# Kernel optimization log

Hardware: AMD Instinct MI355X
Metric: run time of the kernel (lower is better)

## Reference

```python
import jax, jax.numpy as jnp
import numpy as np

PATCH_NUMS = (1, 2, 4, 8, 16)
BETA = 0.25
A = -0.75  # torch bicubic coefficient


def _cubic(s):
    s = abs(s)
    if s <= 1.0:
        return ((A + 2.0) * s - (A + 3.0)) * s * s + 1.0
    if s < 2.0:
        return (((s - 5.0) * s + 8.0) * s - 4.0) * A
    return 0.0


def bicubic_matrix(n_in, n_out):
    # Row-stochastic 1D resampling matrix matching torch upsample_bicubic2d
    # (align_corners=False: half-pixel centers, border index clamping).
    scale = n_in / n_out
    W = np.zeros((n_out, n_in), dtype=np.float32)
    for i in range(n_out):
        x = (i + 0.5) * scale - 0.5
        x0 = int(np.floor(x))
        t = x - x0
        for off in (-1, 0, 1, 2):
            idx = min(max(x0 + off, 0), n_in - 1)
            W[i, idx] += _cubic(t - off)
    return jnp.asarray(W)


def area_down(x, pn):
    # exact average pooling (h, w divisible by pn)
    b, c, h, w = x.shape
    kh, kw = h // pn, w // pn
    return x.reshape(b, c, pn, kh, pn, kw).mean(axis=(3, 5))


def bicubic_up(x, h_out, w_out):
    b, c, h_in, w_in = x.shape
    Wh = bicubic_matrix(h_in, h_out)  # (h_out, h_in)
    Ww = bicubic_matrix(w_in, w_out)  # (w_out, w_in)
    x = jnp.einsum('Oh,bchw->bcOw', Wh, x)
    x = jnp.einsum('Pw,bchw->bchP', Ww, x)
    return x


def vector_quantize(z, embed, beta):
    # z: (b,c,h,w); embed: (V,c)
    b, c, h, w = z.shape
    zf = z.transpose(0, 2, 3, 1).reshape(-1, c)  # (N,c)
    # squared L2 distances to codebook, (N,V)
    d = (zf * zf).sum(-1, keepdims=True) - 2.0 * zf @ embed.T + (embed * embed).sum(-1)
    idx = jnp.argmin(d, axis=1)  # (N,)
    zq = embed[idx].reshape(b, h, w, c).transpose(0, 3, 1, 2)
    sg = jax.lax.stop_gradient
    loss = beta * jnp.mean((sg(zq) - z) ** 2) + jnp.mean((zq - sg(z)) ** 2)
    zq_st = z + sg(zq - z)  # straight-through estimator
    return zq_st, idx.reshape(b, h, w), loss


def setup_inputs() -> dict:
    key = jax.random.key(0)
    k1, k2 = jax.random.split(key)
    z = jax.random.normal(k1, (256, 32, 16, 16), dtype=jnp.float32)
    embed = jax.random.normal(k2, (4096, 32), dtype=jnp.float32)
    return {"z": z, "embed": embed}


def reference(z, embed):
    b, c, h, w = z.shape
    f_rest = z
    f_hat = jnp.zeros_like(z)
    ms_idx = []
    vq_loss = jnp.float32(0.0)
    n = len(PATCH_NUMS)
    for i, pn in enumerate(PATCH_NUMS):
        z_scale = area_down(f_rest, pn) if i < n - 1 else f_rest
        z_q_scale, idx, loss_i = vector_quantize(z_scale, embed, BETA)
        z_q = bicubic_up(z_q_scale, h, w) if i < n - 1 else z_q_scale
        f_hat = f_hat + z_q
        f_rest = f_rest - z_q
        ms_idx.append(idx)
        vq_loss = vq_loss + loss_i
    vq_loss = vq_loss / n
    return (f_hat, *ms_idx, vq_loss)
```

## Files before the change

kernel.cpp:

```cpp
#include <hip/hip_runtime.h>
#include <hip/hip_bf16.h>
#include <cstdint>
#include <cstddef>


#define B_   256
#define V_   4096
#define NTOT 2097152
#define WIN  128
#define CAP  512
#define ZS   65536

using bf16x8 = __attribute__((ext_vector_type(8))) short;
using f32x4  = __attribute__((ext_vector_type(4))) float;

__device__ inline short f2bf(float f) {
  __hip_bfloat16 h = __float2bfloat16(f);
  return *reinterpret_cast<short*>(&h);
}
__device__ inline unsigned encf(float f) {
  unsigned u = __float_as_uint(f);
  return (u & 0x80000000u) ? ~u : (u | 0x80000000u);
}
__device__ inline float decf(unsigned u) {
  unsigned b = (u & 0x80000000u) ? (u ^ 0x80000000u) : ~u;
  return __uint_as_float(b);
}
__device__ inline int keyidx(unsigned long long k) {
  int i = (int)(unsigned)(k & 0xffffffffull);
  return min(max(i, 0), V_ - 1);
}

__global__ __launch_bounds__(256) void setup_kernel(
    const float* __restrict__ z, const float* __restrict__ embed,
    float* __restrict__ f_rest, float* __restrict__ zpack,
    short* __restrict__ ebf, float* __restrict__ se,
    float* __restrict__ tables, float* __restrict__ loss_slots,
    unsigned long long* __restrict__ keys0, unsigned int* __restrict__ smin0)
{
  const int tid = threadIdx.x;
  const int t = blockIdx.x * 256 + tid;
  float v = z[t];
  f_rest[t] = v;

  __shared__ float sm[256];
  sm[tid] = v;
  __syncthreads();
  if (tid == 0) {
    float s = 0.f;
    for (int i = 0; i < 256; ++i) s += sm[i];
    int c = blockIdx.x & 31, b = blockIdx.x >> 5;
    zpack[c * ZS + b] = s * (1.0f / 256.0f);
  }

  if (blockIdx.x < 16) {
    int code = blockIdx.x * 256 + tid;
    float s = 0.f;
#pragma unroll
    for (int c = 0; c < 32; ++c) {
      float e = embed[(size_t)code * 32 + c];
      ebf[(size_t)code * 32 + c] = f2bf(e);
      s += e * e;
    }
    se[code] = s;
  } else if (blockIdx.x == 16) {
    if (tid < 64) {
      int pn_i = tid >> 4;
      int o    = tid & 15;
      int pn   = 1 << pn_i;
      double scale = (double)pn / 16.0;
      double x  = (o + 0.5) * scale - 0.5;
      double x0 = floor(x);
      double tf = x - x0;
      float row[8];
#pragma unroll
      for (int h = 0; h < 8; ++h) row[h] = 0.f;
      const double A = -0.75;
#pragma unroll
      for (int off = -1; off <= 2; ++off) {
        double s = fabs(tf - (double)off);
        double cub;
        if (s <= 1.0)      cub = ((A + 2.0) * s - (A + 3.0)) * s * s + 1.0;
        else if (s < 2.0)  cub = (((s - 5.0) * s + 8.0) * s - 4.0) * A;
        else               cub = 0.0;
        int idx = (int)x0 + off;
        idx = min(max(idx, 0), pn - 1);
        row[idx] = (float)((double)row[idx] + cub);
      }
#pragma unroll
      for (int h = 0; h < 8; ++h) tables[pn_i * 128 + o * 8 + h] = row[h];
    }
  } else if (blockIdx.x == 17) {
    keys0[tid] = ~0ull;
    smin0[tid] = 0xFFFFFFFFu;
  } else if (blockIdx.x >= 20 && blockIdx.x < 60) {
    loss_slots[(blockIdx.x - 20) * 256 + tid] = 0.f;
  }
}

__global__ __launch_bounds__(256) void vq_phaseA_kernel(
    const float* __restrict__ zpack, const short* __restrict__ ebf,
    const float* __restrict__ se, unsigned int* __restrict__ smin,
    int vchunk)
{
  __shared__ __align__(16) short elds[WIN * 40];
  __shared__ float selds[WIN];

  const int tid = threadIdx.x;
  const int lane = tid & 63, wave = tid >> 6;
  const int col = lane & 15, quad = lane >> 4;
  const int nw = blockIdx.x * 128 + wave * 32;
  const int vbase = blockIdx.y * vchunk;

  bf16x8 af[2];
#pragma unroll
  for (int f = 0; f < 2; ++f) {
    const float* zb = zpack + (nw + f * 16 + col);
#pragma unroll
    for (int j = 0; j < 8; ++j)
      af[f][j] = f2bf(-zb[(size_t)(quad * 8 + j) * ZS]);
  }
  float mn[2][4];
#pragma unroll
  for (int f = 0; f < 2; ++f)
#pragma unroll
    for (int r = 0; r < 4; ++r) mn[f][r] = 3.4e38f;

  for (int w0 = 0; w0 < vchunk; w0 += WIN) {
    __syncthreads();
    {
      int row = tid >> 1, half = tid & 1;
      const bf16x8* src = (const bf16x8*)(ebf + (size_t)(vbase + w0 + row) * 32);
      bf16x8* dst = (bf16x8*)(elds + row * 40);
      dst[half * 2]     = src[half * 2];
      dst[half * 2 + 1] = src[half * 2 + 1];
      if (tid < WIN) selds[tid] = 0.5f * se[vbase + w0 + tid];
    }
    __syncthreads();
    for (int vv = 0; vv < WIN; vv += 16) {
      bf16x8 bf = *(const bf16x8*)(elds + (vv + col) * 40 + quad * 8);
      float sevh = selds[vv + col];
      f32x4 cin = {sevh, sevh, sevh, sevh};
#pragma unroll
      for (int f = 0; f < 2; ++f) {
        f32x4 d = __builtin_amdgcn_mfma_f32_16x16x32_bf16(af[f], bf, cin, 0, 0, 0);
#pragma unroll
        for (int r = 0; r < 4; ++r) mn[f][r] = fminf(mn[f][r], d[r]);
      }
    }
  }
#pragma unroll
  for (int f = 0; f < 2; ++f)
#pragma unroll
    for (int r = 0; r < 4; ++r) {
      float m = mn[f][r];
      m = fminf(m, __shfl_xor(m, 1, 64));
      m = fminf(m, __shfl_xor(m, 2, 64));
      m = fminf(m, __shfl_xor(m, 4, 64));
      m = fminf(m, __shfl_xor(m, 8, 64));
      mn[f][r] = m;
    }
  if (col == 0) {
#pragma unroll
    for (int f = 0; f < 2; ++f)
#pragma unroll
      for (int r = 0; r < 4; ++r)
        atomicMin(&smin[nw + f * 16 + quad * 4 + r], encf(mn[f][r]));
  }
}

__global__ __launch_bounds__(256) void vq_phaseB_kernel(
    const float* __restrict__ zpack, const short* __restrict__ ebf,
    const float* __restrict__ se, const unsigned int* __restrict__ smin,
    const float* __restrict__ embed, unsigned long long* __restrict__ keys,
    int vchunk, int nmax)
{
  __shared__ __align__(16) short elds[WIN * 40];
  __shared__ float selds[WIN];
  __shared__ unsigned long long clist[CAP];
  __shared__ int ccnt;

  const int tid = threadIdx.x;
  const int lane = tid & 63, wave = tid >> 6;
  const int col = lane & 15, quad = lane >> 4;
  const int nw = blockIdx.x * 128 + wave * 32;
  const int vbase = blockIdx.y * vchunk;
  const float MARGIN = 1.0f;

  if (tid == 0) ccnt = 0;
  __syncthreads();

  bf16x8 af[2];
#pragma unroll
  for (int f = 0; f < 2; ++f) {
    const float* zb = zpack + (nw + f * 16 + col);
#pragma unroll
    for (int j = 0; j < 8; ++j)
      af[f][j] = f2bf(-zb[(size_t)(quad * 8 + j) * ZS]);
  }
  float thr[2][4];
#pragma unroll
  for (int f = 0; f < 2; ++f)
#pragma unroll
    for (int r = 0; r < 4; ++r)
      thr[f][r] = decf(smin[nw + f * 16 + quad * 4 + r]) + MARGIN;

  for (int w0 = 0; w0 < vchunk; w0 += WIN) {
    __syncthreads();
    {
      int row = tid >> 1, half = tid & 1;
      const bf16x8* src = (const bf16x8*)(ebf + (size_t)(vbase + w0 + row) * 32);
      bf16x8* dst = (bf16x8*)(elds + row * 40);
      dst[half * 2]     = src[half * 2];
      dst[half * 2 + 1] = src[half * 2 + 1];
      if (tid < WIN) selds[tid] = 0.5f * se[vbase + w0 + tid];
    }
    __syncthreads();
    for (int vv = 0; vv < WIN; vv += 16) {
      bf16x8 bf = *(const bf16x8*)(elds + (vv + col) * 40 + quad * 8);
      float sevh = selds[vv + col];
      f32x4 cin = {sevh, sevh, sevh, sevh};
      f32x4 dd[2];
      float hm = 3.4e38f;
#pragma unroll
      for (int f = 0; f < 2; ++f) {
        dd[f] = __builtin_amdgcn_mfma_f32_16x16x32_bf16(af[f], bf, cin, 0, 0, 0);
#pragma unroll
        for (int r = 0; r < 4; ++r) hm = fminf(hm, dd[f][r] - thr[f][r]);
      }
      if (hm <= 0.f) {
#pragma unroll
        for (int f = 0; f < 2; ++f) {
#pragma unroll
          for (int r = 0; r < 4; ++r) {
            if (dd[f][r] <= thr[f][r]) {
              int n = nw + f * 16 + quad * 4 + r;
              int v = vbase + w0 + vv + col;
              int slot = atomicAdd(&ccnt, 1);
              if (slot < CAP) {
                clist[slot] =
                    ((unsigned long long)(unsigned)n << 32) | (unsigned)v;
              } else {
                const float* zp = zpack + n;
                const float* ep = embed + (size_t)v * 32;
                float dot = 0.f, sz = 0.f;
#pragma unroll 1
                for (int i = 0; i < 32; ++i) {
                  float zc = zp[(size_t)i * ZS];
                  dot = fmaf(zc, ep[i], dot);
                  sz  = fmaf(zc, zc, sz);
                }
                float d = fmaf(-2.0f, dot, sz) + se[v];
                unsigned long long key =
                    ((unsigned long long)encf(d) << 32) | (unsigned)v;
                atomicMin(&keys[n], key);
              }
            }
          }
        }
      }
    }
  }

  __syncthreads();
  int tot = min(ccnt, CAP);
  for (int j = tid; j < tot; j += 256) {
    unsigned long long cv = clist[j];
    int n = min((int)(cv >> 32), nmax - 1);
    int v = min((int)(cv & 0xffffffffull), V_ - 1);
    const float* zp = zpack + n;
    const float* ep = embed + (size_t)v * 32;
    float dot = 0.f, sz = 0.f;
#pragma unroll
    for (int i = 0; i < 32; ++i) {
      float zc = zp[(size_t)i * ZS];
      dot = fmaf(zc, ep[i], dot);
      sz  = fmaf(zc, zc, sz);
    }
    float d = fmaf(-2.0f, dot, sz) + se[v];
    unsigned long long key =
        ((unsigned long long)encf(d) << 32) | (unsigned)v;
    atomicMin(&keys[n], key);
  }
}

__global__ __launch_bounds__(256) void up_update_kernel(
    const float* __restrict__ embed, const unsigned long long* __restrict__ keys,
    const float* __restrict__ tbl, float* __restrict__ f_rest, int pn,
    float* __restrict__ zpack_next, unsigned long long* __restrict__ keys_nb,
    unsigned int* __restrict__ smin_nb, int pn_next, int n_next,
    float* __restrict__ idx_out, float* __restrict__ loss_slot)
{
  __shared__ float sm[256];
  __shared__ float sm_e[64];
  const int tid = threadIdx.x;
  const int t = blockIdx.x * 256 + tid;
  const int p = tid & 15, o = tid >> 4;
  const int c = blockIdx.x & 31, b = blockIdx.x >> 5;
  const int pn2 = pn * pn;

  float pre = f_rest[t];
  sm[tid] = pre;
  if (tid < pn2) {
    int idx = keyidx(keys[b * pn2 + tid]);
    if (c == 0) idx_out[b * pn2 + tid] = (float)idx;
    sm_e[tid] = embed[(size_t)idx * 32 + c];
  }
  __syncthreads();

  float lsum = 0.f;
  if (tid < pn2) {
    int k = 16 / pn;
    int ph = tid / pn, pw = tid - ph * pn;
    float s = 0.f;
    for (int i = 0; i < k; ++i)
      for (int j = 0; j < k; ++j)
        s += sm[(ph * k + i) * 16 + (pw * k + j)];
    float zavg = s * (1.0f / (k * k));
    float d = sm_e[tid] - zavg;
    lsum = d * d;
  }
#pragma unroll
  for (int off = 32; off > 0; off >>= 1) lsum += __shfl_down(lsum, off, 64);
  if ((tid & 63) == 0)
    atomicAdd(loss_slot + ((blockIdx.x & 127) << 4), lsum);

  const float* Wo = tbl + o * 8;
  const float* Wp = tbl + p * 8;
  float acc = 0.f;
  for (int w = 0; w < pn; ++w) {
    float inner = 0.f;
    for (int h = 0; h < pn; ++h)
      inner = fmaf(Wo[h], sm_e[h * pn + w], inner);
    acc = fmaf(Wp[w], inner, acc);
  }
  float nr = pre - acc;
  f_rest[t] = nr;

  __syncthreads();
  sm[tid] = nr;
  __syncthreads();
  const int pnn2 = pn_next * pn_next;
  if (tid < pnn2) {
    int ph = tid / pn_next, pw = tid - ph * pn_next;
    int k = 16 / pn_next;
    float s = 0.f;
    for (int i = 0; i < k; ++i)
      for (int j = 0; j < k; ++j)
        s += sm[(ph * k + i) * 16 + (pw * k + j)];
    zpack_next[c * ZS + b * pnn2 + tid] = s * (1.0f / (k * k));
  }
  if (t < n_next) {
    keys_nb[t] = ~0ull;
    smin_nb[t] = 0xFFFFFFFFu;
  }
}

__global__ __launch_bounds__(256) void final_add_kernel(
    const float* __restrict__ z, const float* __restrict__ f_rest,
    const float* __restrict__ embed, const unsigned long long* __restrict__ keys,
    float* __restrict__ f_hat, const float* __restrict__ zpack,
    float* __restrict__ idx_out, float* __restrict__ loss_slot)
{
  const int tid = threadIdx.x;
  const int t = blockIdx.x * 256 + tid;
  const int c = blockIdx.x & 31, b = blockIdx.x >> 5;
  const int n = b * 256 + tid;
  int idx = keyidx(keys[n]);
  if (c == 0) idx_out[n] = (float)idx;
  float e = embed[(size_t)idx * 32 + c];
  f_hat[t] = (z[t] - f_rest[t]) + e;
  float d = e - zpack[c * ZS + n];
  float lsum = d * d;
#pragma unroll
  for (int off = 32; off > 0; off >>= 1) lsum += __shfl_down(lsum, off, 64);
  if ((tid & 63) == 0)
    atomicAdd(loss_slot + ((blockIdx.x & 127) << 4), lsum);
}

__global__ __launch_bounds__(128) void loss_final_kernel(
    const float* __restrict__ loss_slots, float* __restrict__ out_loss)
{
  __shared__ float lred[2];
  const int tid = threadIdx.x;
  const float numel[5] = {8192.f, 32768.f, 131072.f, 524288.f, 2097152.f};
  float tot = 0.f;
  for (int s = 0; s < 5; ++s) {
    float x = loss_slots[s * 2048 + tid * 16];
#pragma unroll
    for (int off = 32; off > 0; off >>= 1) x += __shfl_down(x, off, 64);
    if ((tid & 63) == 0) lred[tid >> 6] = x;
    __syncthreads();
    if (tid == 0) {
      float m = (lred[0] + lred[1]) / numel[s];
      tot += 0.25f * m + m;
    }
    __syncthreads();
  }
  if (tid == 0) out_loss[0] = tot / 5.f;
}

extern "C" void kernel_launch(void* const* d_in, const int* in_sizes, int n_in,
                              void* d_out, int out_size, void* d_ws, size_t ws_size,
                              hipStream_t stream)
{
  const float* z     = (const float*)d_in[0];
  const float* embed = (const float*)d_in[1];
  float* out = (float*)d_out;
  float* ws  = (float*)d_ws;

  float* f_rest = ws;
  float* zpack  = ws + 2097152;
  short* ebf    = (short*)(ws + 4194304);
  float* se     = ws + 4259840;
  unsigned int* smin0 = (unsigned int*)(ws + 4263936);
  unsigned int* smin1 = (unsigned int*)(ws + 4329472);
  unsigned long long* keys0 = (unsigned long long*)(ws + 4345856);
  unsigned long long* keys1 = (unsigned long long*)(ws + 4476928);
  float* loss_slots = ws + 4509696;
  float* tables     = ws + 4519936;

  unsigned long long* keysb[2] = {keys0, keys1};
  unsigned int*       sminb[2] = {smin0, smin1};

  setup_kernel<<<NTOT / 256, 256, 0, stream>>>(z, embed, f_rest, zpack,
                                               ebf, se, tables, loss_slots,
                                               keys0, smin0);

  const int PN[5]  = {1, 2, 4, 8, 16};
  const int NVC[5] = {32, 32, 32, 16, 16};
  int idx_off = NTOT;
  for (int i = 0; i < 5; ++i) {
    int pn = PN[i];
    int N  = B_ * pn * pn;
    int vchunk = V_ / NVC[i];
    unsigned long long* kb = keysb[i & 1];
    unsigned int*       sb = sminb[i & 1];
    dim3 g(N / 128, NVC[i]);
    vq_phaseA_kernel<<<g, 256, 0, stream>>>(zpack, ebf, se, sb, vchunk);
    vq_phaseB_kernel<<<g, 256, 0, stream>>>(zpack, ebf, se, sb, embed, kb,
                                            vchunk, N);
    if (i < 4) {
      int pnn = PN[i + 1];
      up_update_kernel<<<NTOT / 256, 256, 0, stream>>>(
          embed, kb, tables + i * 128, f_rest, pn,
          zpack, keysb[(i + 1) & 1], sminb[(i + 1) & 1],
          pnn, B_ * pnn * pnn, out + idx_off, loss_slots + i * 2048);
    } else {
      final_add_kernel<<<NTOT / 256, 256, 0, stream>>>(
          z, f_rest, embed, kb, out, zpack, out + idx_off,
          loss_slots + 4 * 2048);
    }
    idx_off += N;
  }
  loss_final_kernel<<<1, 128, 0, stream>>>(loss_slots, out + 2184448);
}
```

Measured before the change: 379.8 us.

## Bound phase A on a codebook subset and retune phase B grid splits

```diff
diff --git a/kernel.cpp b/kernel.cpp
--- a/kernel.cpp
+++ b/kernel.cpp
@@ -8,8 +8,9 @@
 #define V_   4096
 #define NTOT 2097152
 #define WIN  128
-#define CAP  512
+#define CAP  1024
 #define ZS   65536
+#define SUBS 1024
 
 using bf16x8 = __attribute__((ext_vector_type(8))) short;
 using f32x4  = __attribute__((ext_vector_type(4))) float;
@@ -29,6 +30,11 @@
 __device__ inline int keyidx(unsigned long long k) {
   int i = (int)(unsigned)(k & 0xffffffffull);
   return min(max(i, 0), V_ - 1);
+}
+__device__ inline float min3f(float a, float b, float c) {
+  float d;
+  asm("v_min3_f32 %0, %1, %2, %3" : "=v"(d) : "v"(a), "v"(b), "v"(c));
+  return d;
 }
 
 __global__ __launch_bounds__(256) void setup_kernel(
@@ -204,6 +210,9 @@
 #pragma unroll
     for (int r = 0; r < 4; ++r)
       thr[f][r] = decf(smin[nw + f * 16 + quad * 4 + r]) + MARGIN;
+  float tmax = fmaxf(
+      fmaxf(fmaxf(thr[0][0], thr[0][1]), fmaxf(thr[0][2], thr[0][3])),
+      fmaxf(fmaxf(thr[1][0], thr[1][1]), fmaxf(thr[1][2], thr[1][3])));
 
   for (int w0 = 0; w0 < vchunk; w0 += WIN) {
     __syncthreads();
@@ -221,14 +230,13 @@
       float sevh = selds[vv + col];
       f32x4 cin = {sevh, sevh, sevh, sevh};
       f32x4 dd[2];
-      float hm = 3.4e38f;
-#pragma unroll
-      for (int f = 0; f < 2; ++f) {
+#pragma unroll
+      for (int f = 0; f < 2; ++f)
         dd[f] = __builtin_amdgcn_mfma_f32_16x16x32_bf16(af[f], bf, cin, 0, 0, 0);
-#pragma unroll
-        for (int r = 0; r < 4; ++r) hm = fminf(hm, dd[f][r] - thr[f][r]);
-      }
-      if (hm <= 0.f) {
+      float m0 = min3f(dd[0][0], dd[0][1], dd[0][2]);
+      float m1 = min3f(dd[0][3], dd[1][0], dd[1][1]);
+      float m2 = min3f(dd[1][2], dd[1][3], m0);
+      if (fminf(m1, m2) <= tmax) {
 #pragma unroll
         for (int f = 0; f < 2; ++f) {
 #pragma unroll
@@ -427,19 +435,21 @@
                                                ebf, se, tables, loss_slots,
                                                keys0, smin0);
 
-  const int PN[5]  = {1, 2, 4, 8, 16};
-  const int NVC[5] = {32, 32, 32, 16, 16};
+  const int PN[5]   = {1, 2, 4, 8, 16};
+  const int NVCA[5] = {8, 8, 8, 4, 2};
+  const int NVCB[5] = {32, 16, 8, 4, 4};
   int idx_off = NTOT;
   for (int i = 0; i < 5; ++i) {
     int pn = PN[i];
     int N  = B_ * pn * pn;
-    int vchunk = V_ / NVC[i];
     unsigned long long* kb = keysb[i & 1];
     unsigned int*       sb = sminb[i & 1];
-    dim3 g(N / 128, NVC[i]);
-    vq_phaseA_kernel<<<g, 256, 0, stream>>>(zpack, ebf, se, sb, vchunk);
-    vq_phaseB_kernel<<<g, 256, 0, stream>>>(zpack, ebf, se, sb, embed, kb,
-                                            vchunk, N);
+    dim3 ga(N / 128, NVCA[i]);
+    vq_phaseA_kernel<<<ga, 256, 0, stream>>>(zpack, ebf, se, sb,
+                                             SUBS / NVCA[i]);
+    dim3 gb(N / 128, NVCB[i]);
+    vq_phaseB_kernel<<<gb, 256, 0, stream>>>(zpack, ebf, se, sb, embed, kb,
+                                             V_ / NVCB[i], N);
     if (i < 4) {
       int pnn = PN[i + 1];
       up_update_kernel<<<NTOT / 256, 256, 0, stream>>>(
```

After: 413.8 us. +8.9%, slower.

## Store averaged z row-major in bf16 and widen VQ waves to 64 rows

Applied to the files above, without the earlier changes.

```diff
diff --git a/kernel.cpp b/kernel.cpp
--- a/kernel.cpp
+++ b/kernel.cpp
@@ -8,8 +8,8 @@
 #define V_   4096
 #define NTOT 2097152
 #define WIN  128
-#define CAP  512
-#define ZS   65536
+#define CAP  1024
+#define MARGIN_ 1.0f
 
 using bf16x8 = __attribute__((ext_vector_type(8))) short;
 using f32x4  = __attribute__((ext_vector_type(4))) float;
@@ -30,13 +30,19 @@
   int i = (int)(unsigned)(k & 0xffffffffull);
   return min(max(i, 0), V_ - 1);
 }
+__device__ inline float min3f(float a, float b, float c) {
+  float d;
+  asm("v_min3_f32 %0, %1, %2, %3" : "=v"(d) : "v"(a), "v"(b), "v"(c));
+  return d;
+}
 
 __global__ __launch_bounds__(256) void setup_kernel(
     const float* __restrict__ z, const float* __restrict__ embed,
-    float* __restrict__ f_rest, float* __restrict__ zpack,
-    short* __restrict__ ebf, float* __restrict__ se,
-    float* __restrict__ tables, float* __restrict__ loss_slots,
-    unsigned long long* __restrict__ keys0, unsigned int* __restrict__ smin0)
+    float* __restrict__ f_rest, float* __restrict__ zrow,
+    short* __restrict__ zrowb, short* __restrict__ ebf,
+    float* __restrict__ se, float* __restrict__ tables,
+    float* __restrict__ loss_slots, unsigned long long* __restrict__ keys0,
+    unsigned int* __restrict__ smin0)
 {
   const int tid = threadIdx.x;
   const int t = blockIdx.x * 256 + tid;
@@ -50,7 +56,9 @@
     float s = 0.f;
     for (int i = 0; i < 256; ++i) s += sm[i];
     int c = blockIdx.x & 31, b = blockIdx.x >> 5;
-    zpack[c * ZS + b] = s * (1.0f / 256.0f);
+    float val = s * (1.0f / 256.0f);
+    zrow[(size_t)b * 32 + c] = val;
+    zrowb[(size_t)b * 32 + c] = f2bf(-val);
   }
 
   if (blockIdx.x < 16) {
@@ -99,7 +107,7 @@
 }
 
 __global__ __launch_bounds__(256) void vq_phaseA_kernel(
-    const float* __restrict__ zpack, const short* __restrict__ ebf,
+    const short* __restrict__ zrowb, const short* __restrict__ ebf,
     const float* __restrict__ se, unsigned int* __restrict__ smin,
     int vchunk)
 {
@@ -109,20 +117,17 @@
   const int tid = threadIdx.x;
   const int lane = tid & 63, wave = tid >> 6;
   const int col = lane & 15, quad = lane >> 4;
-  const int nw = blockIdx.x * 128 + wave * 32;
+  const int nw = blockIdx.x * 256 + wave * 64;
   const int vbase = blockIdx.y * vchunk;
 
-  bf16x8 af[2];
-#pragma unroll
-  for (int f = 0; f < 2; ++f) {
-    const float* zb = zpack + (nw + f * 16 + col);
-#pragma unroll
-    for (int j = 0; j < 8; ++j)
-      af[f][j] = f2bf(-zb[(size_t)(quad * 8 + j) * ZS]);
-  }
-  float mn[2][4];
-#pragma unroll
-  for (int f = 0; f < 2; ++f)
+  bf16x8 af[4];
+#pragma unroll
+  for (int f = 0; f < 4; ++f)
+    af[f] = *(const bf16x8*)(zrowb + (size_t)(nw + f * 16 + col) * 32 + quad * 8);
+
+  float mn[4][4];
+#pragma unroll
+  for (int f = 0; f < 4; ++f)
 #pragma unroll
     for (int r = 0; r < 4; ++r) mn[f][r] = 3.4e38f;
 
@@ -137,20 +142,29 @@
       if (tid < WIN) selds[tid] = 0.5f * se[vbase + w0 + tid];
     }
     __syncthreads();
-    for (int vv = 0; vv < WIN; vv += 16) {
-      bf16x8 bf = *(const bf16x8*)(elds + (vv + col) * 40 + quad * 8);
-      float sevh = selds[vv + col];
-      f32x4 cin = {sevh, sevh, sevh, sevh};
-#pragma unroll
-      for (int f = 0; f < 2; ++f) {
-        f32x4 d = __builtin_amdgcn_mfma_f32_16x16x32_bf16(af[f], bf, cin, 0, 0, 0);
-#pragma unroll
-        for (int r = 0; r < 4; ++r) mn[f][r] = fminf(mn[f][r], d[r]);
-      }
-    }
-  }
-#pragma unroll
-  for (int f = 0; f < 2; ++f)
+#pragma unroll 2
+    for (int vv = 0; vv < WIN; vv += 32) {
+      bf16x8 bfA = *(const bf16x8*)(elds + (vv + col) * 40 + quad * 8);
+      bf16x8 bfB = *(const bf16x8*)(elds + (vv + 16 + col) * 40 + quad * 8);
+      float sa = selds[vv + col], sb = selds[vv + 16 + col];
+      f32x4 cinA = {sa, sa, sa, sa};
+      f32x4 cinB = {sb, sb, sb, sb};
+      f32x4 da[4], db[4];
+#pragma unroll
+      for (int f = 0; f < 4; ++f)
+        da[f] = __builtin_amdgcn_mfma_f32_16x16x32_bf16(af[f], bfA, cinA, 0, 0, 0);
+#pragma unroll
+      for (int f = 0; f < 4; ++f)
+        db[f] = __builtin_amdgcn_mfma_f32_16x16x32_bf16(af[f], bfB, cinB, 0, 0, 0);
+#pragma unroll
+      for (int f = 0; f < 4; ++f)
+#pragma unroll
+        for (int r = 0; r < 4; ++r)
+          mn[f][r] = min3f(mn[f][r], da[f][r], db[f][r]);
+    }
+  }
+#pragma unroll
+  for (int f = 0; f < 4; ++f)
 #pragma unroll
     for (int r = 0; r < 4; ++r) {
       float m = mn[f][r];
@@ -162,7 +176,7 @@
     }
   if (col == 0) {
 #pragma unroll
-    for (int f = 0; f < 2; ++f)
+    for (int f = 0; f < 4; ++f)
 #pragma unroll
       for (int r = 0; r < 4; ++r)
         atomicMin(&smin[nw + f * 16 + quad * 4 + r], encf(mn[f][r]));
@@ -170,10 +184,10 @@
 }
 
 __global__ __launch_bounds__(256) void vq_phaseB_kernel(
-    const float* __restrict__ zpack, const short* __restrict__ ebf,
+    const short* __restrict__ zrowb, const short* __restrict__ ebf,
     const float* __restrict__ se, const unsigned int* __restrict__ smin,
-    const float* __restrict__ embed, unsigned long long* __restrict__ keys,
-    int vchunk, int nmax)
+    const float* __restrict__ zrow, const float* __restrict__ embed,
+    unsigned long long* __restrict__ keys, int vchunk, int nmax)
 {
   __shared__ __align__(16) short elds[WIN * 40];
   __shared__ float selds[WIN];
@@ -183,27 +197,27 @@
   const int tid = threadIdx.x;
   const int lane = tid & 63, wave = tid >> 6;
   const int col = lane & 15, quad = lane >> 4;
-  const int nw = blockIdx.x * 128 + wave * 32;
+  const int nw = blockIdx.x * 256 + wave * 64;
   const int vbase = blockIdx.y * vchunk;
-  const float MARGIN = 1.0f;
 
   if (tid == 0) ccnt = 0;
-  __syncthreads();
-
-  bf16x8 af[2];
-#pragma unroll
-  for (int f = 0; f < 2; ++f) {
-    const float* zb = zpack + (nw + f * 16 + col);
-#pragma unroll
-    for (int j = 0; j < 8; ++j)
-      af[f][j] = f2bf(-zb[(size_t)(quad * 8 + j) * ZS]);
-  }
-  float thr[2][4];
-#pragma unroll
-  for (int f = 0; f < 2; ++f)
+
+  bf16x8 af[4];
+#pragma unroll
+  for (int f = 0; f < 4; ++f)
+    af[f] = *(const bf16x8*)(zrowb + (size_t)(nw + f * 16 + col) * 32 + quad * 8);
+
+  float thr[4][4];
+#pragma unroll
+  for (int f = 0; f < 4; ++f)
 #pragma unroll
     for (int r = 0; r < 4; ++r)
-      thr[f][r] = decf(smin[nw + f * 16 + quad * 4 + r]) + MARGIN;
+      thr[f][r] = decf(smin[nw + f * 16 + quad * 4 + r]) + MARGIN_;
+  float tmax = fmaxf(
+      fmaxf(fmaxf(fmaxf(thr[0][0], thr[0][1]), fmaxf(thr[0][2], thr[0][3])),
+            fmaxf(fmaxf(thr[1][0], thr[1][1]), fmaxf(thr[1][2], thr[1][3]))),
+      fmaxf(fmaxf(fmaxf(thr[2][0], thr[2][1]), fmaxf(thr[2][2], thr[2][3])),
+            fmaxf(fmaxf(thr[3][0], thr[3][1]), fmaxf(thr[3][2], thr[3][3]))));
 
   for (int w0 = 0; w0 < vchunk; w0 += WIN) {
     __syncthreads();
@@ -216,44 +230,65 @@
       if (tid < WIN) selds[tid] = 0.5f * se[vbase + w0 + tid];
     }
     __syncthreads();
-    for (int vv = 0; vv < WIN; vv += 16) {
-      bf16x8 bf = *(const bf16x8*)(elds + (vv + col) * 40 + quad * 8);
-      float sevh = selds[vv + col];
-      f32x4 cin = {sevh, sevh, sevh, sevh};
-      f32x4 dd[2];
-      float hm = 3.4e38f;
-#pragma unroll
-      for (int f = 0; f < 2; ++f) {
-        dd[f] = __builtin_amdgcn_mfma_f32_16x16x32_bf16(af[f], bf, cin, 0, 0, 0);
-#pragma unroll
-        for (int r = 0; r < 4; ++r) hm = fminf(hm, dd[f][r] - thr[f][r]);
-      }
-      if (hm <= 0.f) {
-#pragma unroll
-        for (int f = 0; f < 2; ++f) {
-#pragma unroll
-          for (int r = 0; r < 4; ++r) {
-            if (dd[f][r] <= thr[f][r]) {
-              int n = nw + f * 16 + quad * 4 + r;
-              int v = vbase + w0 + vv + col;
-              int slot = atomicAdd(&ccnt, 1);
-              if (slot < CAP) {
-                clist[slot] =
-                    ((unsigned long long)(unsigned)n << 32) | (unsigned)v;
-              } else {
-                const float* zp = zpack + n;
-                const float* ep = embed + (size_t)v * 32;
-                float dot = 0.f, sz = 0.f;
+#pragma unroll 2
+    for (int vv = 0; vv < WIN; vv += 32) {
+      bf16x8 bfA = *(const bf16x8*)(elds + (vv + col) * 40 + quad * 8);
+      bf16x8 bfB = *(const bf16x8*)(elds + (vv + 16 + col) * 40 + quad * 8);
+      float sa = selds[vv + col], sb = selds[vv + 16 + col];
+      f32x4 cinA = {sa, sa, sa, sa};
+      f32x4 cinB = {sb, sb, sb, sb};
+      f32x4 da[4], db[4];
+#pragma unroll
+      for (int f = 0; f < 4; ++f)
+        da[f] = __builtin_amdgcn_mfma_f32_16x16x32_bf16(af[f], bfA, cinA, 0, 0, 0);
+#pragma unroll
+      for (int f = 0; f < 4; ++f)
+        db[f] = __builtin_amdgcn_mfma_f32_16x16x32_bf16(af[f], bfB, cinB, 0, 0, 0);
+      float m0  = min3f(da[0][0], da[0][1], da[0][2]);
+      float m1  = min3f(da[0][3], da[1][0], da[1][1]);
+      float m2  = min3f(da[1][2], da[1][3], da[2][0]);
+      float m3  = min3f(da[2][1], da[2][2], da[2][3]);
+      float m4  = min3f(da[3][0], da[3][1], da[3][2]);
+      float m5  = min3f(da[3][3], db[0][0], db[0][1]);
+      float m6  = min3f(db[0][2], db[0][3], db[1][0]);
+      float m7  = min3f(db[1][1], db[1][2], db[1][3]);
+      float m8  = min3f(db[2][0], db[2][1], db[2][2]);
+      float m9  = min3f(db[2][3], db[3][0], db[3][1]);
+      float m10 = min3f(db[3][2], db[3][3], m0);
+      float m11 = min3f(m1, m2, m3);
+      float m12 = min3f(m4, m5, m6);
+      float m13 = min3f(m7, m8, m9);
+      float g   = fminf(min3f(m10, m11, m12), m13);
+      if (g <= tmax) {
+#pragma unroll
+        for (int s = 0; s < 2; ++s) {
+#pragma unroll
+          for (int f = 0; f < 4; ++f) {
+#pragma unroll
+            for (int r = 0; r < 4; ++r) {
+              float dv = (s == 0) ? da[f][r] : db[f][r];
+              if (dv <= thr[f][r]) {
+                int n = nw + f * 16 + quad * 4 + r;
+                int v = vbase + w0 + vv + s * 16 + col;
+                int slot = atomicAdd(&ccnt, 1);
+                if (slot < CAP) {
+                  clist[slot] =
+                      ((unsigned long long)(unsigned)n << 32) | (unsigned)v;
+                } else {
+                  const float* zp = zrow + (size_t)n * 32;
+                  const float* ep = embed + (size_t)v * 32;
+                  float dot = 0.f, sz = 0.f;
 #pragma unroll 1
-                for (int i = 0; i < 32; ++i) {
-                  float zc = zp[(size_t)i * ZS];
-                  dot = fmaf(zc, ep[i], dot);
-                  sz  = fmaf(zc, zc, sz);
+                  for (int i = 0; i < 32; ++i) {
+                    float zc = zp[i];
+                    dot = fmaf(zc, ep[i], dot);
+                    sz  = fmaf(zc, zc, sz);
+                  }
+                  float d = fmaf(-2.0f, dot, sz) + se[v];
+                  unsigned long long key =
+                      ((unsigned long long)encf(d) << 32) | (unsigned)v;
+                  atomicMin(&keys[n], key);
                 }
-                float d = fmaf(-2.0f, dot, sz) + se[v];
-                unsigned long long key =
-                    ((unsigned long long)encf(d) << 32) | (unsigned)v;
-                atomicMin(&keys[n], key);
               }
             }
           }
@@ -268,12 +303,12 @@
     unsigned long long cv = clist[j];
     int n = min((int)(cv >> 32), nmax - 1);
     int v = min((int)(cv & 0xffffffffull), V_ - 1);
-    const float* zp = zpack + n;
+    const float* zp = zrow + (size_t)n * 32;
     const float* ep = embed + (size_t)v * 32;
     float dot = 0.f, sz = 0.f;
 #pragma unroll
     for (int i = 0; i < 32; ++i) {
-      float zc = zp[(size_t)i * ZS];
+      float zc = zp[i];
       dot = fmaf(zc, ep[i], dot);
       sz  = fmaf(zc, zc, sz);
     }
@@ -287,8 +322,9 @@
 __global__ __launch_bounds__(256) void up_update_kernel(
     const float* __restrict__ embed, const unsigned long long* __restrict__ keys,
     const float* __restrict__ tbl, float* __restrict__ f_rest, int pn,
-    float* __restrict__ zpack_next, unsigned long long* __restrict__ keys_nb,
-    unsigned int* __restrict__ smin_nb, int pn_next, int n_next,
+    float* __restrict__ zrow, short* __restrict__ zrowb,
+    unsigned long long* __restrict__ keys_nb, unsigned int* __restrict__ smin_nb,
+    int pn_next, int n_next,
     float* __restrict__ idx_out, float* __restrict__ loss_slot)
 {
   __shared__ float sm[256];
@@ -348,7 +384,10 @@
     for (int i = 0; i < k; ++i)
       for (int j = 0; j < k; ++j)
         s += sm[(ph * k + i) * 16 + (pw * k + j)];
-    zpack_next[c * ZS + b * pnn2 + tid] = s * (1.0f / (k * k));
+    float zavg = s * (1.0f / (k * k));
+    size_t nn = (size_t)(b * pnn2 + tid);
+    zrow[nn * 32 + c]  = zavg;
+    zrowb[nn * 32 + c] = f2bf(-zavg);
   }
   if (t < n_next) {
     keys_nb[t] = ~0ull;
@@ -359,8 +398,8 @@
 __global__ __launch_bounds__(256) void final_add_kernel(
     const float* __restrict__ z, const float* __restrict__ f_rest,
     const float* __restrict__ embed, const unsigned long long* __restrict__ keys,
-    float* __restrict__ f_hat, const float* __restrict__ zpack,
-    float* __restrict__ idx_out, float* __restrict__ loss_slot)
+    float* __restrict__ f_hat, float* __restrict__ idx_out,
+    float* __restrict__ loss_slot)
 {
   const int tid = threadIdx.x;
   const int t = blockIdx.x * 256 + tid;
@@ -369,8 +408,9 @@
   int idx = keyidx(keys[n]);
   if (c == 0) idx_out[n] = (float)idx;
   float e = embed[(size_t)idx * 32 + c];
-  f_hat[t] = (z[t] - f_rest[t]) + e;
-  float d = e - zpack[c * ZS + n];
+  float fr = f_rest[t];
+  f_hat[t] = (z[t] - fr) + e;
+  float d = e - fr;
   float lsum = d * d;
 #pragma unroll
   for (int off = 32; off > 0; off >>= 1) lsum += __shfl_down(lsum, off, 64);
@@ -409,21 +449,22 @@
   float* out = (float*)d_out;
   float* ws  = (float*)d_ws;
 
-  float* f_rest = ws;
-  float* zpack  = ws + 2097152;
-  short* ebf    = (short*)(ws + 4194304);
-  float* se     = ws + 4259840;
-  unsigned int* smin0 = (unsigned int*)(ws + 4263936);
-  unsigned int* smin1 = (unsigned int*)(ws + 4329472);
-  unsigned long long* keys0 = (unsigned long long*)(ws + 4345856);
-  unsigned long long* keys1 = (unsigned long long*)(ws + 4476928);
-  float* loss_slots = ws + 4509696;
-  float* tables     = ws + 4519936;
+  float* f_rest  = ws;
+  float* zrow    = ws + 2097152;
+  short* zrowb   = (short*)(ws + 4194304);
+  short* ebf     = (short*)(ws + 5242880);
+  float* se      = ws + 5308416;
+  unsigned int* smin0 = (unsigned int*)(ws + 5312512);
+  unsigned int* smin1 = (unsigned int*)(ws + 5378048);
+  unsigned long long* keys0 = (unsigned long long*)(ws + 5394432);
+  unsigned long long* keys1 = (unsigned long long*)(ws + 5525504);
+  float* loss_slots = ws + 5558272;
+  float* tables     = ws + 5568512;
 
   unsigned long long* keysb[2] = {keys0, keys1};
   unsigned int*       sminb[2] = {smin0, smin1};
 
-  setup_kernel<<<NTOT / 256, 256, 0, stream>>>(z, embed, f_rest, zpack,
+  setup_kernel<<<NTOT / 256, 256, 0, stream>>>(z, embed, f_rest, zrow, zrowb,
                                                ebf, se, tables, loss_slots,
                                                keys0, smin0);
 
@@ -436,20 +477,19 @@
     int vchunk = V_ / NVC[i];
     unsigned long long* kb = keysb[i & 1];
     unsigned int*       sb = sminb[i & 1];
-    dim3 g(N / 128, NVC[i]);
-    vq_phaseA_kernel<<<g, 256, 0, stream>>>(zpack, ebf, se, sb, vchunk);
-    vq_phaseB_kernel<<<g, 256, 0, stream>>>(zpack, ebf, se, sb, embed, kb,
-                                            vchunk, N);
+    dim3 g(N / 256, NVC[i]);
+    vq_phaseA_kernel<<<g, 256, 0, stream>>>(zrowb, ebf, se, sb, vchunk);
+    vq_phaseB_kernel<<<g, 256, 0, stream>>>(zrowb, ebf, se, sb, zrow, embed,
+                                            kb, vchunk, N);
     if (i < 4) {
       int pnn = PN[i + 1];
       up_update_kernel<<<NTOT / 256, 256, 0, stream>>>(
           embed, kb, tables + i * 128, f_rest, pn,
-          zpack, keysb[(i + 1) & 1], sminb[(i + 1) & 1],
+          zrow, zrowb, keysb[(i + 1) & 1], sminb[(i + 1) & 1],
           pnn, B_ * pnn * pnn, out + idx_off, loss_slots + i * 2048);
     } else {
       final_add_kernel<<<NTOT / 256, 256, 0, stream>>>(
-          z, f_rest, embed, kb, out, zpack, out + idx_off,
-          loss_slots + 4 * 2048);
+          z, f_rest, embed, kb, out, out + idx_off, loss_slots + 4 * 2048);
     }
     idx_off += N;
   }
```

Measured after the change: 435.6 us. +14.7%, slower.
